# Optimization experiments

Measured on AMD Instinct MI355X. Metric: run time of the kernel, lower is better.

## Reference

```python
import jax, jax.numpy as jnp
import numpy as np

D_MODEL = 2048
N_HEADS = 16
D_HEAD = D_MODEL // N_HEADS


def setup_inputs() -> dict:
    key = jax.random.key(0)
    ks = jax.random.split(key, 8)
    B, T = 2, 2048
    s = 1.0 / np.sqrt(D_MODEL)
    return {
        "q": jax.random.normal(ks[0], (B, T, D_MODEL), jnp.float32),
        "k": jax.random.normal(ks[1], (B, T, D_MODEL), jnp.float32),
        "v": jax.random.normal(ks[2], (B, T, D_MODEL), jnp.float32),
        "Wq": jax.random.normal(ks[3], (D_MODEL, D_MODEL), jnp.float32) * s,
        "Wk": jax.random.normal(ks[4], (D_MODEL, D_MODEL), jnp.float32) * s,
        "Wv": jax.random.normal(ks[5], (D_MODEL, D_MODEL), jnp.float32) * s,
        "Wo": jax.random.normal(ks[6], (D_MODEL, D_MODEL), jnp.float32) * s,
        "bo": jax.random.normal(ks[7], (D_MODEL,), jnp.float32) * 0.01,
    }


def reference(q, k, v, Wq, Wk, Wv, Wo, bo):
    B, T, C = q.shape
    scale = D_HEAD ** -0.5
    # projections (torch Linear: x @ W.T), split into heads: [B, H, T, Dh]
    qh = (q @ Wq.T).reshape(B, T, N_HEADS, D_HEAD).transpose(0, 2, 1, 3)
    kh = (k @ Wk.T).reshape(B, -1, N_HEADS, D_HEAD).transpose(0, 2, 1, 3)
    vh = (v @ Wv.T).reshape(B, -1, N_HEADS, D_HEAD).transpose(0, 2, 1, 3)
    scores = jnp.einsum("bhqd,bhkd->bhqk", qh, kh) * scale  # [B,H,T,T]
    attn = jax.nn.softmax(scores, axis=-1)
    out = jnp.einsum("bhqk,bhkd->bhqd", attn, vh)  # [B,H,T,Dh]
    out = out.transpose(0, 2, 1, 3).reshape(B, T, C)
    return out @ Wo.T + bo
```

## Files before the change

### kernel.cpp

```cpp
#include <hip/hip_runtime.h>
#include <hip/hip_bf16.h>

typedef unsigned int u32;
typedef unsigned long long u64;
typedef unsigned short u16;
typedef __bf16 bf16_t;
typedef bf16_t bf16x8 __attribute__((ext_vector_type(8)));
typedef float f32x4 __attribute__((ext_vector_type(4)));
typedef float f32x16 __attribute__((ext_vector_type(16)));
typedef float f32x4v __attribute__((ext_vector_type(4)));
typedef u16 u16x8 __attribute__((ext_vector_type(8)));
typedef u32 u32x4 __attribute__((ext_vector_type(4)));

#define GLB __attribute__((address_space(1)))
#define LDSAS __attribute__((address_space(3)))

#define DM 2048
#define NH 16
#define DH 128
#define BB 2
#define TT 2048
#define MT (BB*TT)

static __device__ __forceinline__ u16 f2bf(float f){
    u32 x = __builtin_bit_cast(u32, f);
    return (u16)((x + 0x7FFFu + ((x >> 16) & 1u)) >> 16);
}

static __device__ __forceinline__ f32x4 mfma16(bf16x8 a, bf16x8 b, f32x4 c){
    return __builtin_amdgcn_mfma_f32_16x16x32_bf16(a, b, c, 0, 0, 0);
}

static __device__ __forceinline__ f32x16 mfma32(bf16x8 a, bf16x8 b, f32x16 c){
    return __builtin_amdgcn_mfma_f32_32x32x16_bf16(a, b, c, 0, 0, 0);
}

static __device__ __forceinline__ u32 cvtpk(float lo, float hi){
    u32 r; asm("v_cvt_pk_bf16_f32 %0, %1, %2" : "=v"(r) : "v"(lo), "v"(hi)); return r;
}

static __device__ __forceinline__ void gload_lds16(const u16* g, u16* l){
    __builtin_amdgcn_global_load_lds((const GLB u32*)g, (LDSAS u32*)l, 16, 0, 0);
}

__global__ __launch_bounds__(256) void cast_all(
    const float* __restrict__ q, const float* __restrict__ kin, const float* __restrict__ v,
    const float* __restrict__ wq, const float* __restrict__ wk, const float* __restrict__ wv,
    const float* __restrict__ wo,
    u16* __restrict__ qb, u16* __restrict__ kb, u16* __restrict__ vb,
    u16* __restrict__ wqb, u16* __restrict__ wkb, u16* __restrict__ wvb, u16* __restrict__ wob)
{
    const int QC = MT*DM/8;
    const int WC = DM*DM/8;
    int idx = blockIdx.x*256 + threadIdx.x;
    const float* src; u16* dst; int off;
    if (idx < 3*QC){
        int w = idx / QC; off = idx - w*QC;
        src = (w==0) ? q : (w==1) ? kin : v;
        dst = (w==0) ? qb : (w==1) ? kb : vb;
    } else {
        int j = idx - 3*QC; int w = j / WC; off = j - w*WC;
        src = (w==0) ? wq : (w==1) ? wk : (w==2) ? wv : wo;
        dst = (w==0) ? wqb : (w==1) ? wkb : (w==2) ? wvb : wob;
    }
    const f32x4v* s4 = (const f32x4v*)(src + (u64)off*8);
    f32x4v a = s4[0], b = s4[1];
    u16x8 r;
    r[0]=f2bf(a[0]); r[1]=f2bf(a[1]); r[2]=f2bf(a[2]); r[3]=f2bf(a[3]);
    r[4]=f2bf(b[0]); r[5]=f2bf(b[1]); r[6]=f2bf(b[2]); r[7]=f2bf(b[3]);
    *(u16x8*)(dst + (u64)off*8) = r;
}

template<int MODE>
__global__ __launch_bounds__(256) void gemm_bt(
    const u16* __restrict__ A0, const u16* __restrict__ B0, void* __restrict__ C0,
    const u16* __restrict__ A1, const u16* __restrict__ B1, void* __restrict__ C1,
    const u16* __restrict__ A2, const u16* __restrict__ B2, void* __restrict__ C2,
    const float* __restrict__ bias)
{
    __shared__ u16 Ash[128*32];
    __shared__ u16 Bsh[128*32];
    const u16 *A, *B; void* C;
    {
        int z = blockIdx.z;
        A = (z==0)?A0:(z==1)?A1:A2;
        B = (z==0)?B0:(z==1)?B1:B2;
        C = (z==0)?C0:(z==1)?C1:C2;
    }
    const int tid = threadIdx.x;
    const int lane = tid & 63;
    const int wave = tid >> 6;
    const int wr = wave >> 1, wc = wave & 1;
    const int g = lane >> 4, r16 = lane & 15;
    const int bm = blockIdx.y, bn = blockIdx.x;

    int srow[2], scol[2];
    #pragma unroll
    for (int rd = 0; rd < 2; rd++){
        int i = rd*256 + tid;
        int row = i >> 2;
        int c = (i & 3) ^ ((row >> 1) & 3);
        srow[rd] = row; scol[rd] = c*8;
    }
    const u16* Ag = A + (u64)(bm*128)*DM;
    const u16* Bg = B + (u64)(bn*128)*DM;

    int aoff[4], boff[4];
    #pragma unroll
    for (int mi = 0; mi < 4; mi++){
        int row = wr*64 + mi*16 + r16;
        int c = g ^ ((row >> 1) & 3);
        aoff[mi] = row*32 + c*8;
    }
    #pragma unroll
    for (int ni = 0; ni < 4; ni++){
        int row = wc*64 + ni*16 + r16;
        int c = g ^ ((row >> 1) & 3);
        boff[ni] = row*32 + c*8;
    }

    f32x4 acc[4][4] = {};

    for (int k0 = 0; k0 < DM; k0 += 32){
        #pragma unroll
        for (int rd = 0; rd < 2; rd++){
            int i = rd*256 + tid;
            gload_lds16(Ag + (u64)srow[rd]*DM + k0 + scol[rd], Ash + i*8);
            gload_lds16(Bg + (u64)srow[rd]*DM + k0 + scol[rd], Bsh + i*8);
        }
        __syncthreads();
        bf16x8 af[4], bfr[4];
        #pragma unroll
        for (int mi = 0; mi < 4; mi++) af[mi] = *(const bf16x8*)(Ash + aoff[mi]);
        #pragma unroll
        for (int ni = 0; ni < 4; ni++) bfr[ni] = *(const bf16x8*)(Bsh + boff[ni]);
        #pragma unroll
        for (int mi = 0; mi < 4; mi++)
            #pragma unroll
            for (int ni = 0; ni < 4; ni++)
                acc[mi][ni] = mfma16(af[mi], bfr[ni], acc[mi][ni]);
        __syncthreads();
    }

    #pragma unroll
    for (int mi = 0; mi < 4; mi++){
        #pragma unroll
        for (int ni = 0; ni < 4; ni++){
            int row0 = bm*128 + wr*64 + mi*16 + 4*g;
            int col  = bn*128 + wc*64 + ni*16 + r16;
            if (MODE == 0){
                u16* Cp = (u16*)C;
                #pragma unroll
                for (int rr = 0; rr < 4; rr++)
                    Cp[(u64)(row0+rr)*DM + col] = f2bf(acc[mi][ni][rr]);
            } else {
                float* Cp = (float*)C;
                float bv = bias[col];
                #pragma unroll
                for (int rr = 0; rr < 4; rr++)
                    Cp[(u64)(row0+rr)*DM + col] = acc[mi][ni][rr] + bv;
            }
        }
    }
}

__global__ __launch_bounds__(256) void transpose_v(
    const u16* __restrict__ Vh, u16* __restrict__ Vt)
{
    __shared__ u16 tile[64*80];
    int t0 = blockIdx.x*64, d0 = blockIdx.y*64, bh = blockIdx.z;
    int b = bh >> 4, h = bh & 15;
    int tid = threadIdx.x;
    #pragma unroll
    for (int rd = 0; rd < 2; rd++){
        int i = rd*256 + tid;
        int row = i >> 3, c = i & 7;
        u16x8 vv = *(const u16x8*)(Vh + (u64)(b*TT + t0 + row)*DM + h*DH + d0 + c*8);
        *(u16x8*)(tile + row*80 + c*8) = vv;
    }
    __syncthreads();
    #pragma unroll
    for (int rd = 0; rd < 2; rd++){
        int i = rd*256 + tid;
        int d = i >> 3, tc = (i & 7)*8;
        u16x8 vv;
        #pragma unroll
        for (int j = 0; j < 8; j++) vv[j] = tile[(tc + j)*80 + d];
        *(u16x8*)(Vt + (u64)(bh*DH + d0 + d)*TT + t0 + tc) = vv;
    }
}

static __device__ __forceinline__ void stage_kv(
    const u16* __restrict__ Kbase, const u16* __restrict__ Vbase,
    u16* ksh, u16* vsh, int tid)
{
    #pragma unroll
    for (int rd = 0; rd < 2; rd++){
        int ci = rd*512 + tid;
        int row = ci >> 4, ch = (ci & 15) ^ (row & 7);
        gload_lds16(Kbase + (u64)row*DM + ch*8, ksh + ci*8);
    }
    #pragma unroll
    for (int rd = 0; rd < 2; rd++){
        int ci = rd*512 + tid;
        int row = ci >> 3, ch = (ci & 7) ^ (row & 7);
        gload_lds16(Vbase + (u64)row*TT + ch*8, vsh + ci*8);
    }
}

__global__ __launch_bounds__(512, 2) void flash_attn2(
    const u16* __restrict__ Qh, const u16* __restrict__ Kh,
    const u16* __restrict__ Vt, u16* __restrict__ Ao)
{
    __shared__ __align__(16) u16 Ksh[2][64*128];
    __shared__ __align__(16) u16 Vsh[2][128*64];
    __shared__ __align__(16) float asc[8][32];

    const int f = blockIdx.x + 8*(blockIdx.y + 16*blockIdx.z);
    const int qt = f >> 5, bhl = f & 31;
    const int b = bhl >> 4, h = bhl & 15;
    const int bh = b*NH + h;

    const int tid = threadIdx.x, lane = tid & 63, wave = tid >> 6;
    const int l31 = lane & 31, hi = lane >> 5, l7 = lane & 7;
    const float scale = 0.08838834764831845f;

    bf16x8 qf[8];
    {
        const u16* qp = Qh + (u64)(b*TT + qt*256 + wave*32 + l31)*DM + h*DH + hi*8;
        #pragma unroll
        for (int c = 0; c < 8; c++) qf[c] = *(const bf16x8*)(qp + c*16);
    }

    const u16* Kb = Kh + (u64)(b*TT)*DM + h*DH;
    const u16* Vb = Vt + (u64)bh*DH*TT;

    f32x16 accO[4] = {};
    float m_ = -1e30f, l_ = 0.f;

    stage_kv(Kb, Vb, Ksh[0], Vsh[0], tid);
    __syncthreads();

    for (int it = 0; it < TT/64; it++){
        const int cur = it & 1;
        if (it < TT/64 - 1)
            stage_kv(Kb + (u64)(it+1)*64*DM, Vb + (it+1)*64,
                     Ksh[cur^1], Vsh[cur^1], tid);

        f32x16 s0 = {}, s1 = {};
        #pragma unroll
        for (int c = 0; c < 8; c++){
            int ch = (2*c + hi) ^ l7;
            bf16x8 k0 = *(const bf16x8*)(Ksh[cur] + l31*128 + ch*8);
            bf16x8 k1 = *(const bf16x8*)(Ksh[cur] + (32 + l31)*128 + ch*8);
            s0 = mfma32(k0, qf[c], s0);
            s1 = mfma32(k1, qf[c], s1);
        }

        float pe[32];
        #pragma unroll
        for (int r = 0; r < 16; r++){ pe[r] = s0[r]*scale; pe[16+r] = s1[r]*scale; }
        float mx = pe[0];
        #pragma unroll
        for (int i = 1; i < 32; i++) mx = fmaxf(mx, pe[i]);
        mx = fmaxf(mx, __shfl_xor(mx, 32));
        float mnew = fmaxf(m_, mx);
        float alpha = __expf(m_ - mnew);
        m_ = mnew;
        float ls = 0.f;
        #pragma unroll
        for (int i = 0; i < 32; i++){ pe[i] = __expf(pe[i] - mnew); ls += pe[i]; }
        ls += __shfl_xor(ls, 32);
        l_ = l_*alpha + ls;

        if (lane < 32) asc[wave][l31] = alpha;
        f32x4 av[4];
        #pragma unroll
        for (int j = 0; j < 4; j++) av[j] = *(const f32x4*)&asc[wave][8*j + 4*hi];
        #pragma unroll
        for (int dt = 0; dt < 4; dt++)
            #pragma unroll
            for (int r = 0; r < 16; r++)
                accO[dt][r] *= av[r>>2][r&3];

        bf16x8 pa[4];
        #pragma unroll
        for (int c = 0; c < 4; c++){
            u32 a0 = cvtpk(pe[8*c+0], pe[8*c+1]);
            u32 b0 = cvtpk(pe[8*c+4], pe[8*c+5]);
            u32 a1 = cvtpk(pe[8*c+2], pe[8*c+3]);
            u32 b1 = cvtpk(pe[8*c+6], pe[8*c+7]);
            asm volatile("v_permlane32_swap_b32 %0, %1" : "+v"(a0), "+v"(b0));
            asm volatile("v_permlane32_swap_b32 %0, %1" : "+v"(a1), "+v"(b1));
            u32x4 w = {a0, a1, b0, b1};
            pa[c] = __builtin_bit_cast(bf16x8, w);
        }

        #pragma unroll
        for (int dt = 0; dt < 4; dt++){
            #pragma unroll
            for (int c = 0; c < 4; c++){
                int ch = (2*c + hi) ^ l7;
                bf16x8 vf = *(const bf16x8*)(Vsh[cur] + (32*dt + l31)*64 + ch*8);
                accO[dt] = mfma32(pa[c], vf, accO[dt]);
            }
        }
        __syncthreads();
    }

    float linv = 1.f / l_;
    if (lane < 32) asc[wave][l31] = linv;
    f32x4 lv[4];
    #pragma unroll
    for (int j = 0; j < 4; j++) lv[j] = *(const f32x4*)&asc[wave][8*j + 4*hi];
    #pragma unroll
    for (int dt = 0; dt < 4; dt++){
        #pragma unroll
        for (int r = 0; r < 16; r++){
            int qrow = (r&3) + 8*(r>>2) + 4*hi;
            int grow = b*TT + qt*256 + wave*32 + qrow;
            int gcol = h*DH + 32*dt + l31;
            Ao[(u64)grow*DM + gcol] = f2bf(accO[dt][r] * lv[r>>2][r&3]);
        }
    }
}

extern "C" void kernel_launch(void* const* d_in, const int* in_sizes, int n_in,
                              void* d_out, int out_size, void* d_ws, size_t ws_size,
                              hipStream_t stream)
{
    const float* q  = (const float*)d_in[0];
    const float* k  = (const float*)d_in[1];
    const float* v  = (const float*)d_in[2];
    const float* wq = (const float*)d_in[3];
    const float* wk = (const float*)d_in[4];
    const float* wv = (const float*)d_in[5];
    const float* wo = (const float*)d_in[6];
    const float* bo = (const float*)d_in[7];
    float* out = (float*)d_out;

    const u64 SZQ = (u64)MT*DM;
    const u64 SZW = (u64)DM*DM;
    u16* ws  = (u16*)d_ws;
    u16* qb  = ws;
    u16* kb  = ws + SZQ;
    u16* vb  = ws + 2*SZQ;
    u16* wqb = ws + 3*SZQ;
    u16* wkb = wqb + SZW;
    u16* wvb = wqb + 2*SZW;
    u16* wob = wqb + 3*SZW;
    u16* qh  = ws + 5*SZQ;
    u16* kh  = ws + 6*SZQ;
    u16* vh  = ws + 7*SZQ;
    u16* vt  = qb;
    u16* ao  = vb;

    cast_all<<<dim3(20480), dim3(256), 0, stream>>>(
        q, k, v, wq, wk, wv, wo, qb, kb, vb, wqb, wkb, wvb, wob);

    gemm_bt<0><<<dim3(16, 32, 3), dim3(256), 0, stream>>>(
        qb, wqb, qh, kb, wkb, kh, vb, wvb, vh, nullptr);

    transpose_v<<<dim3(32, 2, 32), dim3(256), 0, stream>>>(vh, vt);

    flash_attn2<<<dim3(8, 16, 2), dim3(512), 0, stream>>>(qh, kh, vt, ao);

    gemm_bt<1><<<dim3(16, 32, 1), dim3(256), 0, stream>>>(
        ao, wob, (void*)out, ao, wob, (void*)out, ao, wob, (void*)out, bo);
}
```

Baseline: 441.7 us.

## Rewrite projection GEMMs with 256x128 tiles and triple-buffered LDS pipeline

Replaces the single-buffered 128x128 GEMM with an 8-wave kernel using 256x128 output tiles, a K step of 64, and a three-stage LDS ring. Global-to-LDS loads for tile t+2 are interleaved with the MFMA work on tile t, with vmcnt waits, s_setprio and split barriers. The goal is to hide global load latency and cut barrier stalls. The cost is 144KB of LDS per block, which limits occupancy, and a more fragile schedule.

After: 435.3 us. Within noise of the previous version (-1.4%).

```diff
diff --git a/kernel.cpp b/kernel.cpp
--- a/kernel.cpp
+++ b/kernel.cpp
@@ -72,14 +72,14 @@
 }
 
 template<int MODE>
-__global__ __launch_bounds__(256) void gemm_bt(
+__global__ __launch_bounds__(512, 2) void gemm8p(
     const u16* __restrict__ A0, const u16* __restrict__ B0, void* __restrict__ C0,
     const u16* __restrict__ A1, const u16* __restrict__ B1, void* __restrict__ C1,
     const u16* __restrict__ A2, const u16* __restrict__ B2, void* __restrict__ C2,
     const float* __restrict__ bias)
 {
-    __shared__ u16 Ash[128*32];
-    __shared__ u16 Bsh[128*32];
+    __shared__ __align__(16) u16 lds[3*24576];
+
     const u16 *A, *B; void* C;
     {
         int z = blockIdx.z;
@@ -90,64 +90,105 @@
     const int tid = threadIdx.x;
     const int lane = tid & 63;
     const int wave = tid >> 6;
-    const int wr = wave >> 1, wc = wave & 1;
+    const int wm = wave >> 1, wn = wave & 1;
     const int g = lane >> 4, r16 = lane & 15;
     const int bm = blockIdx.y, bn = blockIdx.x;
 
-    int srow[2], scol[2];
-    #pragma unroll
-    for (int rd = 0; rd < 2; rd++){
-        int i = rd*256 + tid;
-        int row = i >> 2;
-        int c = (i & 3) ^ ((row >> 1) & 3);
-        srow[rd] = row; scol[rd] = c*8;
-    }
-    const u16* Ag = A + (u64)(bm*128)*DM;
+    const u16* Ag = A + (u64)(bm*256)*DM;
     const u16* Bg = B + (u64)(bn*128)*DM;
 
-    int aoff[4], boff[4];
+    const int srow8 = (tid >> 3) & 7;
+    const int sch   = (tid & 7) ^ srow8;
+    const u16* Asrc = Ag + (u64)(tid >> 3)*DM + sch*8;
+    const u16* Bsrc = Bg + (u64)(tid >> 3)*DM + sch*8;
+
+    #define STAGE_A(buf, t2, c) gload_lds16(Asrc + (u64)(c)*64*DM + (t2)*64, (buf) + (c)*4096 + tid*8)
+    #define STAGE_B(buf, t2, c) gload_lds16(Bsrc + (u64)(c)*64*DM + (t2)*64, (buf) + 16384 + (c)*4096 + tid*8)
+
+    int aoff[4][2], boff[4][2];
+    #pragma unroll
+    for (int mi = 0; mi < 4; mi++)
+        #pragma unroll
+        for (int kk = 0; kk < 2; kk++){
+            int row = wm*64 + mi*16 + r16;
+            aoff[mi][kk] = row*64 + (((4*kk + g) ^ (r16 & 7))*8);
+        }
+    #pragma unroll
+    for (int ni = 0; ni < 4; ni++)
+        #pragma unroll
+        for (int kk = 0; kk < 2; kk++){
+            int row = wn*64 + ni*16 + r16;
+            boff[ni][kk] = 16384 + row*64 + (((4*kk + g) ^ (r16 & 7))*8);
+        }
+
+    f32x4 acc[4][4] = {};
+    const int NT = DM/64;
+
+    #pragma unroll
+    for (int c = 0; c < 4; c++) STAGE_A(lds, 0, c);
+    #pragma unroll
+    for (int c = 0; c < 2; c++) STAGE_B(lds, 0, c);
+    #pragma unroll
+    for (int c = 0; c < 4; c++) STAGE_A(lds + 24576, 1, c);
+    #pragma unroll
+    for (int c = 0; c < 2; c++) STAGE_B(lds + 24576, 1, c);
+    asm volatile("s_waitcnt vmcnt(6)" ::: "memory");
+    __builtin_amdgcn_s_barrier();
+    __builtin_amdgcn_sched_barrier(0);
+
+    int cb = 0;
+    for (int t = 0; t < NT; ++t){
+        const u16* bufc = lds + cb*24576;
+        int sb = cb + 2; if (sb >= 3) sb -= 3;
+        u16* bufs = lds + sb*24576;
+        const bool st = (t + 2) < NT;
+
+        #pragma unroll
+        for (int q = 0; q < 4; ++q){
+            const int qm = q >> 1, qn = q & 1;
+            bf16x8 af[2][2], bff[2][2];
+            #pragma unroll
+            for (int i = 0; i < 2; i++)
+                #pragma unroll
+                for (int kk = 0; kk < 2; kk++){
+                    af[i][kk]  = *(const bf16x8*)(bufc + aoff[2*qm + i][kk]);
+                    bff[i][kk] = *(const bf16x8*)(bufc + boff[2*qn + i][kk]);
+                }
+            if (st){
+                if (q == 0){ STAGE_A(bufs, t+2, 0); STAGE_A(bufs, t+2, 1); }
+                else if (q == 1){ STAGE_A(bufs, t+2, 2); STAGE_A(bufs, t+2, 3); }
+                else if (q == 2){ STAGE_B(bufs, t+2, 0); }
+                else            { STAGE_B(bufs, t+2, 1); }
+            }
+            __builtin_amdgcn_s_barrier();
+            __builtin_amdgcn_s_setprio(1);
+            #pragma unroll
+            for (int i = 0; i < 2; i++)
+                #pragma unroll
+                for (int j = 0; j < 2; j++)
+                    #pragma unroll
+                    for (int kk = 0; kk < 2; kk++)
+                        acc[2*qm + i][2*qn + j] =
+                            mfma16(af[i][kk], bff[j][kk], acc[2*qm + i][2*qn + j]);
+            __builtin_amdgcn_s_setprio(0);
+            if (q == 3){
+                if (st)              asm volatile("s_waitcnt vmcnt(6)" ::: "memory");
+                else if (t + 1 < NT) asm volatile("s_waitcnt vmcnt(0)" ::: "memory");
+            }
+            __builtin_amdgcn_s_barrier();
+            if (q == 3) __builtin_amdgcn_sched_barrier(0);
+        }
+        cb = cb + 1; if (cb >= 3) cb = 0;
+    }
+    #undef STAGE_A
+    #undef STAGE_B
+
     #pragma unroll
     for (int mi = 0; mi < 4; mi++){
-        int row = wr*64 + mi*16 + r16;
-        int c = g ^ ((row >> 1) & 3);
-        aoff[mi] = row*32 + c*8;
-    }
-    #pragma unroll
-    for (int ni = 0; ni < 4; ni++){
-        int row = wc*64 + ni*16 + r16;
-        int c = g ^ ((row >> 1) & 3);
-        boff[ni] = row*32 + c*8;
-    }
-
-    f32x4 acc[4][4] = {};
-
-    for (int k0 = 0; k0 < DM; k0 += 32){
-        #pragma unroll
-        for (int rd = 0; rd < 2; rd++){
-            int i = rd*256 + tid;
-            gload_lds16(Ag + (u64)srow[rd]*DM + k0 + scol[rd], Ash + i*8);
-            gload_lds16(Bg + (u64)srow[rd]*DM + k0 + scol[rd], Bsh + i*8);
-        }
-        __syncthreads();
-        bf16x8 af[4], bfr[4];
-        #pragma unroll
-        for (int mi = 0; mi < 4; mi++) af[mi] = *(const bf16x8*)(Ash + aoff[mi]);
-        #pragma unroll
-        for (int ni = 0; ni < 4; ni++) bfr[ni] = *(const bf16x8*)(Bsh + boff[ni]);
-        #pragma unroll
-        for (int mi = 0; mi < 4; mi++)
-            #pragma unroll
-            for (int ni = 0; ni < 4; ni++)
-                acc[mi][ni] = mfma16(af[mi], bfr[ni], acc[mi][ni]);
-        __syncthreads();
-    }
-
-    #pragma unroll
-    for (int mi = 0; mi < 4; mi++){
         #pragma unroll
         for (int ni = 0; ni < 4; ni++){
-            int row0 = bm*128 + wr*64 + mi*16 + 4*g;
-            int col  = bn*128 + wc*64 + ni*16 + r16;
+            int row0 = bm*256 + wm*64 + mi*16 + 4*g;
+            int col  = bn*128 + wn*64 + ni*16 + r16;
             if (MODE == 0){
                 u16* Cp = (u16*)C;
                 #pragma unroll
@@ -358,13 +399,13 @@
     cast_all<<<dim3(20480), dim3(256), 0, stream>>>(
         q, k, v, wq, wk, wv, wo, qb, kb, vb, wqb, wkb, wvb, wob);
 
-    gemm_bt<0><<<dim3(16, 32, 3), dim3(256), 0, stream>>>(
+    gemm8p<0><<<dim3(16, 16, 3), dim3(512), 0, stream>>>(
         qb, wqb, qh, kb, wkb, kh, vb, wvb, vh, nullptr);
 
     transpose_v<<<dim3(32, 2, 32), dim3(256), 0, stream>>>(vh, vt);
 
     flash_attn2<<<dim3(8, 16, 2), dim3(512), 0, stream>>>(qh, kh, vt, ao);
 
-    gemm_bt<1><<<dim3(16, 32, 1), dim3(256), 0, stream>>>(
+    gemm8p<1><<<dim3(16, 16, 1), dim3(512), 0, stream>>>(
         ao, wob, (void*)out, ao, wob, (void*)out, ao, wob, (void*)out, bo);
 }
```
